# Optimization experiments

Measured on AMD Instinct MI355X. Metric: run time of the kernel, lower is better.

The kernel has to match this reference:

```python
import jax, jax.numpy as jnp
import numpy as np

N = 100000; S = 8; V = 10000; DE = 64; DH = 64; H = DH + 6; T = 2; E = 250000
MAXP = 10; SZ = 64; OUT = MAXP * SZ; NPLAIN = 6; NAR = 2


def setup_inputs() -> dict:
    key = jax.random.key(0)
    ks = jax.random.split(key, 20)
    rn = lambda k, sh, s=0.1: jax.random.normal(k, sh, jnp.float32) * s
    return {
        "tokens": jax.random.randint(ks[0], (N, S), 0, V, jnp.int32),
        "type_idx": jax.random.randint(ks[1], (N,), 0, 6, jnp.int32),
        "edge_src": jax.random.randint(ks[2], (T, E), 0, N, jnp.int32),
        "edge_dst": jax.random.randint(ks[3], (T, E), 0, N, jnp.int32),
        "map_entry_idx": 123,
        "embed": rn(ks[4], (V, DE), 0.3),
        "Wi_map": rn(ks[5], (3 * DH, DE)), "Wh_map": rn(ks[6], (3 * DH, DH)),
        "bi_map": jnp.zeros((3 * DH,), jnp.float32), "bh_map": jnp.zeros((3 * DH,), jnp.float32),
        "Wi_mem": rn(ks[7], (3 * DH, DE)), "Wh_mem": rn(ks[8], (3 * DH, DH)),
        "bi_mem": jnp.zeros((3 * DH,), jnp.float32), "bh_mem": jnp.zeros((3 * DH,), jnp.float32),
        "Wm_plain": rn(ks[9], (NPLAIN, T, H, H)), "bm_plain": jnp.zeros((NPLAIN, T, H), jnp.float32),
        "Wu_plain": rn(ks[10], (NPLAIN, 2 * H, H)), "bu_plain": jnp.zeros((NPLAIN, H), jnp.float32),
        "Wm_ar": rn(ks[11], (NAR, T, 2 * H, 2 * H)), "bm_ar": jnp.zeros((NAR, T, 2 * H), jnp.float32),
        "Wu_ar": rn(ks[12], (NAR, 4 * H, H)), "bu_ar": jnp.zeros((NAR, H), jnp.float32),
        "W1": rn(ks[13], (H, H)), "b1": jnp.zeros((H,), jnp.float32),
        "W2": rn(ks[14], (H, OUT)), "b2": jnp.zeros((OUT,), jnp.float32),
    }


def _gru_last(x_seq, Wi, Wh, bi, bh):
    # x_seq: [S, N, DE] -> last hidden [N, DH] (torch nn.GRU cell math)
    def step(h, x):
        gi = x @ Wi.T + bi
        gh = h @ Wh.T + bh
        ir, iz, inn = jnp.split(gi, 3, axis=-1)
        hr, hz, hn = jnp.split(gh, 3, axis=-1)
        r = jax.nn.sigmoid(ir + hr)
        z = jax.nn.sigmoid(iz + hz)
        n = jnp.tanh(inn + r * hn)
        return (1.0 - z) * n + z * h, None
    h0 = jnp.zeros((x_seq.shape[1], Wh.shape[1]), x_seq.dtype)
    h, _ = jax.lax.scan(step, h0, x_seq)
    return h


def _mp(h, src, dst, Wm, bm, Wu, bu, msg_act, dense_act):
    # per-edge-type linear message on sender state, scatter-max aggregation, dense update
    m = jnp.einsum('ted,tdm->tem', h[src], Wm) + bm[:, None, :]  # [T, E, M]
    if msg_act is not None:
        m = msg_act(m)
    agg = jax.ops.segment_max(m.reshape(-1, m.shape[-1]), dst.reshape(-1), num_segments=h.shape[0])
    agg = jnp.where(jnp.isneginf(agg), 0.0, agg)  # nodes with no incoming edges -> 0
    u = jnp.concatenate([h, agg], axis=-1) @ Wu + bu
    return dense_act(u) if dense_act is not None else u


def _forward(tokens, type_idx, edge_src, edge_dst, map_entry_idx, embed,
             Wi_map, Wh_map, bi_map, bh_map, Wi_mem, Wh_mem, bi_mem, bh_mem,
             Wm_plain, bm_plain, Wu_plain, bu_plain, Wm_ar, bm_ar, Wu_ar, bu_ar,
             W1, b1, W2, b2):
    x_seq = embed[tokens].transpose(1, 0, 2)  # [S, N, DE]
    h_map = _gru_last(x_seq, Wi_map, Wh_map, bi_map, bh_map)
    h_mem = _gru_last(x_seq, Wi_mem, Wh_mem, bi_mem, bh_mem)
    is_map = (type_idx == 0)[:, None]
    is_mem = (type_idx == 5)[:, None]
    node_h = jnp.where(is_map, h_map, jnp.where(is_mem, h_mem, 0.0))
    h = jnp.concatenate([jax.nn.one_hot(type_idx, 6, dtype=node_h.dtype), node_h], axis=-1)  # [N, H]
    li = 0
    for blk in range(2):  # two concat-residual blocks from create_mlp_mp_layers
        saved = h
        for _ in range(3):  # plain MLP MP layers: no msg/dense activation
            h = _mp(h, edge_src, edge_dst, Wm_plain[li], bm_plain[li], Wu_plain[li], bu_plain[li], None, None)
            li += 1
        h = jnp.concatenate([saved, h], axis=-1)  # ConcatResidualLayer -> [N, 2H]
        h = _mp(h, edge_src, edge_dst, Wm_ar[blk], bm_ar[blk], Wu_ar[blk], bu_ar[blk], jax.nn.gelu, jnp.tanh)
    x = h[map_entry_idx]            # select map entry node
    x = jax.nn.relu(x @ W1 + b1)    # trans_layers[0]
    return x @ W2 + b2


def reference(tokens, type_idx, edge_src, edge_dst, map_entry_idx, embed,
              Wi_map, Wh_map, bi_map, bh_map, Wi_mem, Wh_mem, bi_mem, bh_mem,
              Wm_plain, bm_plain, Wu_plain, bu_plain, Wm_ar, bm_ar, Wu_ar, bu_ar,
              W1, b1, W2, b2):
    return _forward(tokens, type_idx, edge_src, edge_dst, map_entry_idx, embed,
                    Wi_map, Wh_map, bi_map, bh_map, Wi_mem, Wh_mem, bi_mem, bh_mem,
                    Wm_plain, bm_plain, Wu_plain, bu_plain, Wm_ar, bm_ar, Wu_ar, bu_ar,
                    W1, b1, W2, b2)
```

## Files before the change

kernel.cpp:

```cpp
#include <hip/hip_runtime.h>
#include <math.h>

#define CAPT 20480
#define R2   (2*CAPT)
#define GLD  136
#define GRR  32

typedef __attribute__((ext_vector_type(8))) short short8;
typedef __attribute__((ext_vector_type(4))) float f32x4;

__device__ __forceinline__ float fexp2_(float x){ return __builtin_amdgcn_exp2f(x); }
__device__ __forceinline__ float frcp_(float x){ return __builtin_amdgcn_rcpf(x); }
__device__ __forceinline__ float ftanh_(float x){
  float ax = __builtin_fabsf(x);
  float t = fexp2_(-2.885390082f * ax);
  float r = (1.f - t) * frcp_(1.f + t);
  return __builtin_copysignf(r, x);
}
__device__ __forceinline__ float fsig_(float x){
  return frcp_(1.f + fexp2_(-1.442695041f * x));
}
__device__ __forceinline__ float fgelu_(float x){
  float x2 = x*x;
  float u  = x * __builtin_fmaf(x2, 0.044715f, 1.0f);
  float e  = fexp2_(u * -2.30220818f);
  return x * frcp_(1.f + e);
}
__device__ __forceinline__ unsigned short f2bf(float x){
  unsigned int u = __float_as_uint(x);
  return (unsigned short)((u + 0x7FFFu + ((u>>16)&1u)) >> 16);
}
__device__ __forceinline__ float bf2f(unsigned short v){
  return __uint_as_float(((unsigned int)v) << 16);
}
__device__ __forceinline__ unsigned int cvt_pk_bf16(float a, float b){
  unsigned int r;
  asm("v_cvt_pk_bf16_f32 %0, %1, %2" : "=v"(r) : "v"(a), "v"(b));
  return r;
}

__global__ void k_prepB(const float* __restrict__ Wm_plain, const float* __restrict__ Wu_plain,
                        const float* __restrict__ Wm_ar, const float* __restrict__ Wu_ar,
                        const float* __restrict__ Wi_map, const float* __restrict__ Wh_map,
                        const float* __restrict__ Wi_mem, const float* __restrict__ Wh_mem,
                        unsigned short* __restrict__ BtArena){
  int id = blockIdx.y;
  int Kp, elems, off;
  if (id < 6){ Kp=96;  elems=15360; off=id*15360; }
  else if (id < 12){ Kp=160; elems=12800; off=92160+(id-6)*12800; }
  else if (id < 14){ Kp=160; elems=51200; off=168960+(id-12)*51200; }
  else if (id < 16){ Kp=320; elems=25600; off=271360+(id-14)*25600; }
  else { Kp=128; elems=32768; off=322560+(id-16)*32768; }
  for (int g = blockIdx.x*256 + threadIdx.x; g < elems; g += 8*256){
    int c = g / Kp, k = g - c*Kp;
    float val = 0.f;
    if (id < 6){
      int li = id; int t = (c >= 80); int cc = c - t*80;
      if (cc < 70 && k < 70) val = Wm_plain[((li*2+t)*70 + k)*70 + cc];
    } else if (id < 12){
      int li = id-6;
      int kk = (k < 70) ? k : ((k >= 80 && k < 150) ? 70 + (k-80) : -1);
      if (c < 70 && kk >= 0) val = Wu_plain[(li*140 + kk)*70 + c];
    } else if (id < 14){
      int blk = id-12; int t = (c >= 160); int cc = c - t*160;
      int kk = (k < 70) ? k : ((k >= 80 && k < 150) ? 70 + (k-80) : -1);
      if (cc < 140 && kk >= 0) val = Wm_ar[(((blk*2+t)*140) + kk)*140 + cc];
    } else if (id < 16){
      int blk = id-14;
      int kk = (k < 70) ? k : ((k >= 80 && k < 150) ? 70 + (k-80)
               : ((k >= 160 && k < 300) ? 140 + (k-160) : -1));
      if (c < 70 && kk >= 0) val = Wu_ar[(blk*280 + kk)*70 + c];
    } else {
      int typ = id-16;
      const float* Wi = typ ? Wi_mem : Wi_map;
      const float* Wh = typ ? Wh_mem : Wh_map;
      if (c < 192) val = (k < 64) ? Wi[c*64 + k] : Wh[c*64 + (k-64)];
      else { int cc = c-192; val = (k >= 64) ? Wh[(128+cc)*64 + (k-64)] : 0.f; }
    }
    BtArena[off + g] = f2bf(val);
  }
}

__global__ void k_prepBias(const float* __restrict__ bm_plain, const float* __restrict__ bu_plain,
                           const float* __restrict__ bm_ar, const float* __restrict__ bu_ar,
                           const float* __restrict__ bi_map, const float* __restrict__ bh_map,
                           const float* __restrict__ bi_mem, const float* __restrict__ bh_mem,
                           float* __restrict__ biasA){
  for (int g = threadIdx.x; g < 2752; g += 256){
    float val = 0.f;
    if (g < 960){ int li=g/160, c=g%160; int t=(c>=80); int cc=c-t*80;
      if (cc<70) val = bm_plain[(li*2+t)*70 + cc]; }
    else if (g < 1440){ int u=g-960; int li=u/80, c=u%80; if (c<70) val = bu_plain[li*70+c]; }
    else if (g < 2080){ int u=g-1440; int blk=u/320, c=u%320; int t=(c>=160); int cc=c-t*160;
      if (cc<140) val = bm_ar[(blk*2+t)*140 + cc]; }
    else if (g < 2240){ int u=g-2080; int blk=u/80, c=u%80; if (c<70) val = bu_ar[blk*70+c]; }
    else { int u=g-2240; int typ=u/256, c=u%256;
      const float* bi = typ ? bi_mem : bi_map; const float* bh = typ ? bh_mem : bh_map;
      val = (c < 192) ? (bi[c]+bh[c]) : bh[128 + (c-192)]; }
    biasA[g] = val;
  }
}

__global__ void k_prepEmb(const float* __restrict__ embed, unsigned short* __restrict__ embB,
                          int total){
  int g = blockIdx.x*256 + threadIdx.x;
  if (g < total) embB[g] = f2bf(embed[g]);
}

__global__ void k_init_h(const int* __restrict__ type_idx, unsigned short* __restrict__ h, int N){
  int g = blockIdx.x*256 + threadIdx.x;
  if (g >= N*80) return;
  int n = g / 80, c = g - n*80;
  h[g] = (c < 6 && type_idx[n] == c) ? (unsigned short)0x3F80 : (unsigned short)0;
}

__global__ void k_compact(const int* __restrict__ type_idx, int* __restrict__ idxcat,
                          int* __restrict__ cnt, int N){
  int n = blockIdx.x*256 + threadIdx.x;
  if (n >= N) return;
  int t = type_idx[n];
  if (t == 0){ int p = atomicAdd(&cnt[0],1); if (p < CAPT) idxcat[p] = n; }
  else if (t == 5){ int p = atomicAdd(&cnt[1],1); if (p < CAPT) idxcat[CAPT+p] = n; }
}

__global__ void k_count(const int* __restrict__ edst, int* __restrict__ deg, int TE){
  int i = blockIdx.x*256 + threadIdx.x;
  if (i < TE) atomicAdd(&deg[edst[i]], 1);
}
__global__ void k_scan1(const int* __restrict__ deg, int* __restrict__ off,
                        int* __restrict__ bsum, int N){
  __shared__ int sh[256];
  int t = threadIdx.x; int base = blockIdx.x*2048;
  int v[8]; int s = 0;
  for (int i=0;i<8;i++){
    int g = base + t*8 + i;
    int x = (g<N)? (((deg[g]+3)>>2)<<2) : 0;
    v[i]=x; s+=x;
  }
  sh[t]=s; __syncthreads();
  for (int o=1;o<256;o<<=1){ int x = (t>=o)? sh[t-o]:0; __syncthreads(); sh[t]+=x; __syncthreads(); }
  if (t==255) bsum[blockIdx.x] = sh[255];
  int run = sh[t]-s;
  for (int i=0;i<8;i++){ int g = base + t*8 + i; if (g<N) off[g]=run; run+=v[i]; }
}
__global__ void k_scan2(int* bsum, int nb){
  if (threadIdx.x==0 && blockIdx.x==0){
    int run=0;
    for(int b=0;b<nb;b++){ int x=bsum[b]; bsum[b]=run; run+=x; }
    bsum[nb]=run;
  }
}
__global__ void k_scan3(int* __restrict__ off, const int* __restrict__ bsum, int N, int nb){
  int g = blockIdx.x*256+threadIdx.x;
  if (g < N) off[g] += bsum[g>>11];
  if (g == 0) off[N] = bsum[nb];
}
__global__ void k_fill(const int* __restrict__ esrc, const int* __restrict__ edst,
                       const int* __restrict__ off, int* __restrict__ cur,
                       int* __restrict__ edata, int TE, int E){
  int i = blockIdx.x*256 + threadIdx.x;
  if (i >= TE) return;
  int d = edst[i];
  int pos = off[d] + atomicAdd(&cur[d], 1);
  edata[pos] = (esrc[i] << 1) | (i >= E ? 1 : 0);
}
__global__ void k_pad(const int* __restrict__ off, const int* __restrict__ cur,
                      int* __restrict__ edata, int N){
  int n = blockIdx.x*256 + threadIdx.x;
  if (n >= N) return;
  int d = cur[n];
  if (d == 0) return;
  int d4 = ((d+3)>>2)<<2;
  int base = off[n];
  int first = edata[base];
  for (int i = d; i < d4; i++) edata[base+i] = first;
}

__global__ __launch_bounds__(256) void kgru(
    const int* __restrict__ idxcat, const int* __restrict__ tokens,
    const unsigned short* __restrict__ embB,
    const unsigned short* __restrict__ Bt, const unsigned short* __restrict__ Bt2,
    const float* __restrict__ bias, const float* __restrict__ bias2,
    unsigned short* __restrict__ hOut)
{
  __shared__ __align__(16) unsigned short As[2][GRR*GLD];
  __shared__ int tokS[GRR*8];
  __shared__ int idxS[GRR];
  int rb = blockIdx.y * CAPT + blockIdx.x * GRR;
  if (idxcat[rb] < 0) return;
  int t = threadIdx.x;
  int lane = t & 63, m = lane & 15, q = lane >> 4, w = t >> 6;
  const unsigned short* Bsel = blockIdx.y ? Bt2 : Bt;
  const float* bsel = blockIdx.y ? bias2 : bias;
  short8 breg[4][4]; float bv[4];
  #pragma unroll
  for (int j=0;j<4;j++){
    int col = (w + 4*j)*16 + m;
    bv[j] = bsel[col];
    #pragma unroll
    for (int kt=0;kt<4;kt++)
      breg[j][kt] = *(const short8*)&Bsel[(size_t)col*128 + kt*32 + q*8];
  }
  if (t < GRR) idxS[t] = idxcat[rb + t];
  if (t < GRR*8){
    int nd = idxcat[rb + (t>>3)]; if (nd < 0) nd = 0;
    tokS[t] = tokens[nd*8 + (t & 7)];
  }
  __syncthreads();
  if (t < GRR*8){
    int row = t >> 3, ch = t & 7;
    *(uint4*)&As[0][row*GLD + ch*8] = *(const uint4*)&embB[(size_t)tokS[row*8]*64 + ch*8];
  }
  for (int j = t; j < GRR*32; j += 256){
    int row = j >> 5, k2 = (j & 31)*2;
    *(unsigned int*)&As[0][row*GLD + 64 + k2] = 0;
  }
  __syncthreads();
  unsigned short hreg[2][4];
  #pragma unroll
  for (int rt=0;rt<2;rt++)
    #pragma unroll
    for (int i=0;i<4;i++) hreg[rt][i] = 0;
  int u = w*16 + m;
  int p = 0;
  for (int s = 0; s < 8; s++){
    uint4 xr;
    if (s < 7 && t < GRR*8){
      int row = t >> 3, ch = t & 7;
      xr = *(const uint4*)&embB[(size_t)tokS[row*8 + s + 1]*64 + ch*8];
    }
    f32x4 acc[2][4] = {};
    #pragma unroll
    for (int kt=0;kt<4;kt++){
      short8 af[2];
      #pragma unroll
      for (int rt=0;rt<2;rt++)
        af[rt] = *(const short8*)&As[p][(rt*16+m)*GLD + kt*32 + q*8];
      #pragma unroll
      for (int j=0;j<4;j++)
        #pragma unroll
        for (int rt=0;rt<2;rt++)
          acc[rt][j] = __builtin_amdgcn_mfma_f32_16x16x32_bf16(af[rt], breg[j][kt], acc[rt][j], 0,0,0);
    }
    #pragma unroll
    for (int rt=0;rt<2;rt++){
      float hv[4];
      #pragma unroll
      for (int i=0;i<4;i++){
        float rr = fsig_(acc[rt][0][i] + bv[0]);
        float zz = fsig_(acc[rt][1][i] + bv[1]);
        float hn = acc[rt][3][i] + bv[3];
        float nn = ftanh_(acc[rt][2][i] + bv[2] + (rr - 1.f)*hn);
        float hp = bf2f(hreg[rt][i]);
        hv[i] = (1.f - zz)*nn + zz*hp;
      }
      unsigned int plo = cvt_pk_bf16(hv[0], hv[1]);
      unsigned int phi = cvt_pk_bf16(hv[2], hv[3]);
      hreg[rt][0] = (unsigned short)plo;
      hreg[rt][1] = (unsigned short)(plo >> 16);
      hreg[rt][2] = (unsigned short)phi;
      hreg[rt][3] = (unsigned short)(phi >> 16);
    }
    if (s < 7){
      #pragma unroll
      for (int rt=0;rt<2;rt++)
        #pragma unroll
        for (int i=0;i<4;i++)
          As[p^1][(rt*16 + q*4 + i)*GLD + 64 + u] = hreg[rt][i];
      if (t < GRR*8){
        int row = t >> 3, ch = t & 7;
        *(uint4*)&As[p^1][row*GLD + ch*8] = xr;
      }
      __syncthreads();
      p ^= 1;
    } else {
      #pragma unroll
      for (int rt=0;rt<2;rt++)
        #pragma unroll
        for (int i=0;i<4;i++){
          int nd = idxS[rt*16 + q*4 + i];
          if (nd >= 0) hOut[(size_t)nd*80 + 6 + u] = hreg[rt][i];
        }
    }
  }
}

template<int RTR, int KT, int CT, int ACT>
__global__ __launch_bounds__(256) void wgemm(
    const unsigned short* __restrict__ A0, int w0, int ldA0,
    const unsigned short* __restrict__ A1, int w1, int ldA1,
    const unsigned short* __restrict__ A2, int w2, int ldA2,
    const unsigned short* __restrict__ Bt, int KpB,
    const float* __restrict__ bias,
    unsigned short* __restrict__ C, int ldC,
    int rows, int tiles)
{
  constexpr int Kpad = KT*32;
  constexpr int NRT  = RTR/16;
  constexpr int CPT  = (RTR*Kpad/8)/256;
  __shared__ __align__(16) unsigned short As[2][RTR*Kpad];
  int t = threadIdx.x;
  int lane = t & 63, m = lane & 15, q = lane >> 4, w = t >> 6;
  int tileBase = blockIdx.y * (4*CT);
  int rtEnd = (rows + RTR - 1)/RTR;
  int tr = blockIdx.x;
  if (tr >= rtEnd) return;

  short8 breg[CT][KT]; float bv[CT]; bool val[CT]; int colr[CT];
  #pragma unroll
  for (int j=0;j<CT;j++){
    int tt = tileBase + w + 4*j;
    val[j] = (tt < tiles);
    int col = tt*16 + m;
    colr[j] = col;
    bv[j] = 0.f;
    if (val[j]){
      bv[j] = bias[col];
      #pragma unroll
      for (int kt=0;kt<KT;kt++)
        breg[j][kt] = *(const short8*)&Bt[(size_t)col*KpB + kt*32 + q*8];
    } else {
      #pragma unroll
      for (int kt=0;kt<KT;kt++) breg[j][kt] = (short8){0,0,0,0,0,0,0,0};
    }
  }

  int w01 = w0 + w1, w012 = w0 + w1 + w2;
  uint4 r[CPT];
  auto loadRegs = [&](int trr){
    #pragma unroll
    for (int i=0;i<CPT;i++){
      int c = i*256 + t;
      int row = c / (KT*4), kc = (c - row*(KT*4))*8;
      int gr = trr*RTR + row;
      uint4 v = {0,0,0,0};
      if (gr < rows && kc < w012){
        const unsigned short* sp;
        if (kc < w0)       sp = A0 + (size_t)gr*ldA0 + kc;
        else if (kc < w01) sp = A1 + (size_t)gr*ldA1 + (kc - w0);
        else               sp = A2 + (size_t)gr*ldA2 + (kc - w01);
        v = *(const uint4*)sp;
      }
      r[i] = v;
    }
  };
  auto dsw = [&](int p){
    #pragma unroll
    for (int i=0;i<CPT;i++){
      int c = i*256 + t;
      int row = c / (KT*4), ch = c - row*(KT*4);
      int phys = ch ^ (row & 3);
      *(uint4*)&As[p][row*Kpad + phys*8] = r[i];
    }
  };

  loadRegs(tr);
  dsw(0);
  int p = 0;
  for (;;){
    int nxt = tr + gridDim.x;
    bool hasNext = (nxt < rtEnd);
    if (hasNext) loadRegs(nxt);
    __syncthreads();
    f32x4 acc[NRT][CT] = {};
    #pragma unroll
    for (int kt=0;kt<KT;kt++){
      short8 af[NRT];
      #pragma unroll
      for (int rt=0;rt<NRT;rt++)
        af[rt] = *(const short8*)&As[p][(rt*16+m)*Kpad + (((kt*4+q) ^ (m&3))*8)];
      #pragma unroll
      for (int j=0;j<CT;j++)
        #pragma unroll
        for (int rt=0;rt<NRT;rt++)
          acc[rt][j] = __builtin_amdgcn_mfma_f32_16x16x32_bf16(af[rt], breg[j][kt], acc[rt][j], 0,0,0);
    }
    bool tfull = (tr*RTR + RTR <= rows);
#define EPILOG(CHK)                                                         \
    _Pragma("unroll")                                                       \
    for (int rt=0;rt<NRT;rt++){                                             \
      int rbase = tr*RTR + rt*16 + q*4;                                     \
      _Pragma("unroll")                                                     \
      for (int j=0;j<CT;j++){                                               \
        if (!val[j]) continue;                                              \
        float v0 = acc[rt][j][0] + bv[j];                                   \
        float v1 = acc[rt][j][1] + bv[j];                                   \
        float v2 = acc[rt][j][2] + bv[j];                                   \
        float v3 = acc[rt][j][3] + bv[j];                                   \
        if (ACT == 1){ v0=fgelu_(v0); v1=fgelu_(v1); v2=fgelu_(v2); v3=fgelu_(v3); } \
        else if (ACT == 2){ v0=ftanh_(v0); v1=ftanh_(v1); v2=ftanh_(v2); v3=ftanh_(v3); } \
        unsigned int plo = cvt_pk_bf16(v0, v1);                             \
        unsigned int phi = cvt_pk_bf16(v2, v3);                             \
        size_t cb = (size_t)rbase*ldC + colr[j];                            \
        if (!CHK || rbase+0 < rows) C[cb]           = (unsigned short)plo;         \
        if (!CHK || rbase+1 < rows) C[cb + ldC]     = (unsigned short)(plo >> 16); \
        if (!CHK || rbase+2 < rows) C[cb + 2*ldC]   = (unsigned short)phi;         \
        if (!CHK || rbase+3 < rows) C[cb + 3*ldC]   = (unsigned short)(phi >> 16); \
      }                                                                     \
    }
    if (tfull){ EPILOG(false) } else { EPILOG(true) }
#undef EPILOG
    if (!hasNext) break;
    dsw(p^1);
    p ^= 1; tr = nxt;
  }
}

__global__ __launch_bounds__(256) void k_aggregate(
    const int* __restrict__ off, const int* __restrict__ edata,
    const unsigned short* __restrict__ P2, int ldP, int off1,
    unsigned short* __restrict__ agg, int M, int N, int WPN)
{
  int t = threadIdx.x;
  int lane = t & 63, w = t >> 6;
  int nbase, c;
  if (WPN == 1){
    nbase = blockIdx.x*16 + w*4;
    c = 2*lane;
  } else {
    nbase = blockIdx.x*8 + (w>>1)*4;
    c = (w & 1)*80 + 2*lane;
  }
  nbase = __builtin_amdgcn_readfirstlane(nbase);
  if (nbase >= N) return;
  bool act = (lane < 40);
  const float NEG = -__builtin_inff();
  int e[4], e1[4];
  float f0[4], f1[4];
  #pragma unroll
  for (int j=0;j<4;j++){
    int n = nbase + j;
    bool v = (n < N);
    e[j]  = v ? __builtin_amdgcn_readfirstlane(off[n])     : 0;
    e1[j] = v ? __builtin_amdgcn_readfirstlane(off[n + 1]) : 0;
    f0[j] = NEG; f1[j] = NEG;
  }
  for (;;){
    bool cond[4];
    bool any = false;
    #pragma unroll
    for (int j=0;j<4;j++){ cond[j] = (e[j] < e1[j]); any |= cond[j]; }
    if (!any) break;
    unsigned int rr[4][4];
    #pragma unroll
    for (int j=0;j<4;j++){
      if (cond[j]){
        int4 g = *(const int4*)&edata[e[j]];
        int b0 = (g.x>>1)*ldP + (g.x&1)*off1;
        int b1 = (g.y>>1)*ldP + (g.y&1)*off1;
        int b2 = (g.z>>1)*ldP + (g.z&1)*off1;
        int b3 = (g.w>>1)*ldP + (g.w&1)*off1;
        if (act){
          rr[j][0] = *(const unsigned int*)(P2 + b0 + c);
          rr[j][1] = *(const unsigned int*)(P2 + b1 + c);
          rr[j][2] = *(const unsigned int*)(P2 + b2 + c);
          rr[j][3] = *(const unsigned int*)(P2 + b3 + c);
        }
      }
    }
    #pragma unroll
    for (int j=0;j<4;j++){
      if (cond[j]){
        if (act){
          unsigned int u0 = rr[j][0], u1 = rr[j][1], u2 = rr[j][2], u3 = rr[j][3];
          f0[j] = fmaxf(f0[j], fmaxf(fmaxf(__uint_as_float(u0<<16), __uint_as_float(u1<<16)),
                                     fmaxf(__uint_as_float(u2<<16), __uint_as_float(u3<<16))));
          f1[j] = fmaxf(f1[j], fmaxf(fmaxf(__uint_as_float(u0&0xFFFF0000u), __uint_as_float(u1&0xFFFF0000u)),
                                     fmaxf(__uint_as_float(u2&0xFFFF0000u), __uint_as_float(u3&0xFFFF0000u))));
        }
        e[j] += 4;
      }
    }
  }
  if (act){
    #pragma unroll
    for (int j=0;j<4;j++){
      int n = nbase + j;
      if (n >= N) continue;
      unsigned int o = (__float_as_uint(f0[j] == NEG ? 0.f : f0[j]) >> 16)
                     |  (__float_as_uint(f1[j] == NEG ? 0.f : f1[j]) & 0xFFFF0000u);
      *(unsigned int*)(agg + (size_t)n*M + c) = o;
    }
  }
}

__global__ void k_head(const unsigned short* __restrict__ h, const int* __restrict__ entry,
                       const float* __restrict__ W1, const float* __restrict__ b1,
                       const float* __restrict__ W2, const float* __restrict__ b2,
                       float* __restrict__ out){
  __shared__ float x[70], x1[70];
  int t = threadIdx.x;
  if (t < 70) x[t] = bf2f(h[(size_t)(*entry)*80 + t]);
  __syncthreads();
  if (t < 70){
    float s = b1[t];
    for (int i=0;i<70;i++) s += x[i]*W1[i*70 + t];
    x1[t] = fmaxf(s, 0.f);
  }
  __syncthreads();
  if (t < 640){
    float s = b2[t];
    for (int i=0;i<70;i++) s += x1[i]*W2[i*640 + t];
    out[t] = s;
  }
}

extern "C" void kernel_launch(void* const* d_in, const int* in_sizes, int n_in,
                              void* d_out, int out_size, void* d_ws, size_t ws_size,
                              hipStream_t stream) {
  const int*   tokens   = (const int*)d_in[0];
  const int*   type_idx = (const int*)d_in[1];
  const int*   esrc     = (const int*)d_in[2];
  const int*   edst     = (const int*)d_in[3];
  const int*   entry    = (const int*)d_in[4];
  const float* embed    = (const float*)d_in[5];
  const float* Wi_map   = (const float*)d_in[6];
  const float* Wh_map   = (const float*)d_in[7];
  const float* bi_map   = (const float*)d_in[8];
  const float* bh_map   = (const float*)d_in[9];
  const float* Wi_mem   = (const float*)d_in[10];
  const float* Wh_mem   = (const float*)d_in[11];
  const float* bi_mem   = (const float*)d_in[12];
  const float* bh_mem   = (const float*)d_in[13];
  const float* Wm_plain = (const float*)d_in[14];
  const float* bm_plain = (const float*)d_in[15];
  const float* Wu_plain = (const float*)d_in[16];
  const float* bu_plain = (const float*)d_in[17];
  const float* Wm_ar    = (const float*)d_in[18];
  const float* bm_ar    = (const float*)d_in[19];
  const float* Wu_ar    = (const float*)d_in[20];
  const float* bu_ar    = (const float*)d_in[21];
  const float* W1 = (const float*)d_in[22];
  const float* b1 = (const float*)d_in[23];
  const float* W2 = (const float*)d_in[24];
  const float* b2 = (const float*)d_in[25];
  float* out = (float*)d_out;

  const int N  = in_sizes[1];
  const int TE = in_sizes[2];
  const int E  = TE / 2;
  const int V64 = in_sizes[5];

  char* p = (char*)d_ws;
  auto alloc = [&](size_t bytes)->char* { char* r = p; p += (bytes + 255) & ~(size_t)255; return r; };
  unsigned short* hA  = (unsigned short*)alloc((size_t)N*80*2);
  unsigned short* hB  = (unsigned short*)alloc((size_t)N*80*2);
  unsigned short* hC  = (unsigned short*)alloc((size_t)N*80*2);
  unsigned short* P2  = (unsigned short*)alloc((size_t)N*320*2);
  unsigned short* agg = (unsigned short*)alloc((size_t)N*160*2);
  int* deg    = (int*)alloc((size_t)N*4);
  int* curp   = (int*)alloc((size_t)N*4);
  int* off    = (int*)alloc((size_t)(N+8)*4);
  int* edata  = (int*)alloc((size_t)(TE + 4*N + 16)*4);
  int* sbsum  = (int*)alloc(256*4);
  int* cnt    = (int*)alloc(16*4);
  int* idxcat = (int*)alloc((size_t)R2*4);
  unsigned short* BtA  = (unsigned short*)alloc(388096*2);
  float* biasA = (float*)alloc(2752*4);
  unsigned short* embB = (unsigned short*)alloc((size_t)V64*2);

  hipMemsetAsync(idxcat, 0xFF, (size_t)R2*4, stream);
  hipMemsetAsync(cnt,    0,    16*4, stream);
  hipMemsetAsync(deg,    0,    (size_t)N*4, stream);
  hipMemsetAsync(curp,   0,    (size_t)N*4, stream);

  k_prepB<<<dim3(8,18), 256, 0, stream>>>(Wm_plain, Wu_plain, Wm_ar, Wu_ar,
                                          Wi_map, Wh_map, Wi_mem, Wh_mem, BtA);
  k_prepBias<<<1, 256, 0, stream>>>(bm_plain, bu_plain, bm_ar, bu_ar,
                                    bi_map, bh_map, bi_mem, bh_mem, biasA);
  k_prepEmb<<<(V64+255)/256, 256, 0, stream>>>(embed, embB, V64);
  k_init_h<<<(N*80+255)/256, 256, 0, stream>>>(type_idx, hA, N);
  k_compact<<<(N+255)/256, 256, 0, stream>>>(type_idx, idxcat, cnt, N);

  k_count<<<(TE+255)/256, 256, 0, stream>>>(edst, deg, TE);
  int nb = (N + 2047)/2048;
  k_scan1<<<nb, 256, 0, stream>>>(deg, off, sbsum, N);
  k_scan2<<<1, 64, 0, stream>>>(sbsum, nb);
  k_scan3<<<(N+255)/256, 256, 0, stream>>>(off, sbsum, N, nb);
  k_fill<<<(TE+255)/256, 256, 0, stream>>>(esrc, edst, off, curp, edata, TE, E);
  k_pad<<<(N+255)/256, 256, 0, stream>>>(off, curp, edata, N);

  kgru<<<dim3(CAPT/GRR, 2), 256, 0, stream>>>(
      idxcat, tokens, embB,
      BtA + 322560, BtA + 322560 + 32768,
      biasA + 2240, biasA + 2240 + 256, hA);

  unsigned short* cur = hA; unsigned short* f1 = hB; unsigned short* f2 = hC;
  int li = 0;
  for (int blk = 0; blk < 2; blk++){
    unsigned short* saved = cur;
    unsigned short* ins[3]  = {cur, f1, f2};
    unsigned short* outs[3] = {f1, f2, f1};
    for (int j = 0; j < 3; j++){
      unsigned short* X = ins[j]; unsigned short* Yo = outs[j];
      wgemm<64,3,3,0><<<dim3(1024,1), 256, 0, stream>>>(
          X, 80, 80,  nullptr, 0, 0,  nullptr, 0, 0,
          BtA + li*15360, 96, biasA + li*160,
          P2, 160, N, 10);
      k_aggregate<<<(N+15)/16, 256, 0, stream>>>(off, edata, P2, 160, 80, agg, 80, N, 1);
      wgemm<64,5,2,0><<<dim3(1024,1), 256, 0, stream>>>(
          X, 80, 80,  agg, 80, 80,  nullptr, 0, 0,
          BtA + 92160 + li*12800, 160, biasA + 960 + li*80,
          Yo, 80, N, 5);
      li++;
    }
    wgemm<64,5,3,1><<<dim3(512,2), 256, 0, stream>>>(
        saved, 80, 80,  f1, 80, 80,  nullptr, 0, 0,
        BtA + 168960 + blk*51200, 160, biasA + 1440 + blk*320,
        P2, 320, N, 20);
    k_aggregate<<<(N+7)/8, 256, 0, stream>>>(off, edata, P2, 320, 160, agg, 160, N, 2);
    wgemm<32,10,2,2><<<dim3(1024,1), 256, 0, stream>>>(
        saved, 80, 80,  f1, 80, 80,  agg, 160, 160,
        BtA + 271360 + blk*25600, 320, biasA + 2080 + blk*80,
        f2, 80, N, 5);
    unsigned short* t3 = cur; cur = f2; f2 = t3;
  }

  k_head<<<1, 640, 0, stream>>>(cur, entry, W1, b1, W2, b2, out);
}
```

Before: 760.3 us.

## Replace persistent double-buffered wgemm with one-tile-per-block launch; simplify GRU activations

The wgemm kernels are no longer persistent: instead of a fixed grid looping over row tiles with register prefetch and double-buffered LDS, each block now handles exactly one row tile and the grid is sized to the number of tiles. This removes the loop, the second LDS buffer and the prefetch logic, and relies on hardware scheduling across many more blocks to hide load latency. The cost is reloading the B-weight registers in every block. Separately, tanh is rewritten as 1-2/(1+e^{2x}) and the GRU gate math is reorganised into FMAs with a folded (r-1) term, which removes a few ALU ops but may lose some accuracy or saturate differently for large inputs.

```diff
diff --git a/kernel.cpp b/kernel.cpp
--- a/kernel.cpp
+++ b/kernel.cpp
@@ -12,10 +12,8 @@
 __device__ __forceinline__ float fexp2_(float x){ return __builtin_amdgcn_exp2f(x); }
 __device__ __forceinline__ float frcp_(float x){ return __builtin_amdgcn_rcpf(x); }
 __device__ __forceinline__ float ftanh_(float x){
-  float ax = __builtin_fabsf(x);
-  float t = fexp2_(-2.885390082f * ax);
-  float r = (1.f - t) * frcp_(1.f + t);
-  return __builtin_copysignf(r, x);
+  float t = fexp2_(2.885390082f * x);
+  return __builtin_fmaf(-2.f, frcp_(1.f + t), 1.f);
 }
 __device__ __forceinline__ float fsig_(float x){
   return frcp_(1.f + fexp2_(-1.442695041f * x));
@@ -247,12 +245,16 @@
       float hv[4];
       #pragma unroll
       for (int i=0;i<4;i++){
-        float rr = fsig_(acc[rt][0][i] + bv[0]);
-        float zz = fsig_(acc[rt][1][i] + bv[1]);
-        float hn = acc[rt][3][i] + bv[3];
-        float nn = ftanh_(acc[rt][2][i] + bv[2] + (rr - 1.f)*hn);
+        float xrg = acc[rt][0][i] + bv[0];
+        float xzg = acc[rt][1][i] + bv[1];
+        float xng = acc[rt][2][i] + bv[2];
+        float hng = acc[rt][3][i] + bv[3];
+        float pm = frcp_(1.f + fexp2_(1.442695041f*xrg));
+        float zz = frcp_(1.f + fexp2_(-1.442695041f*xzg));
+        float a  = __builtin_fmaf(-pm, hng, xng);
+        float th = ftanh_(a);
         float hp = bf2f(hreg[rt][i]);
-        hv[i] = (1.f - zz)*nn + zz*hp;
+        hv[i] = __builtin_fmaf(zz, hp - th, th);
       }
       unsigned int plo = cvt_pk_bf16(hv[0], hv[1]);
       unsigned int phi = cvt_pk_bf16(hv[2], hv[3]);
@@ -298,7 +300,7 @@
   constexpr int Kpad = KT*32;
   constexpr int NRT  = RTR/16;
   constexpr int CPT  = (RTR*Kpad/8)/256;
-  __shared__ __align__(16) unsigned short As[2][RTR*Kpad];
+  __shared__ __align__(16) unsigned short As[RTR*Kpad];
   int t = threadIdx.x;
   int lane = t & 63, m = lane & 15, q = lane >> 4, w = t >> 6;
   int tileBase = blockIdx.y * (4*CT);
@@ -327,55 +329,44 @@
 
   int w01 = w0 + w1, w012 = w0 + w1 + w2;
   uint4 r[CPT];
-  auto loadRegs = [&](int trr){
-    #pragma unroll
-    for (int i=0;i<CPT;i++){
-      int c = i*256 + t;
-      int row = c / (KT*4), kc = (c - row*(KT*4))*8;
-      int gr = trr*RTR + row;
-      uint4 v = {0,0,0,0};
-      if (gr < rows && kc < w012){
-        const unsigned short* sp;
-        if (kc < w0)       sp = A0 + (size_t)gr*ldA0 + kc;
-        else if (kc < w01) sp = A1 + (size_t)gr*ldA1 + (kc - w0);
-        else               sp = A2 + (size_t)gr*ldA2 + (kc - w01);
-        v = *(const uint4*)sp;
-      }
-      r[i] = v;
-    }
-  };
-  auto dsw = [&](int p){
-    #pragma unroll
-    for (int i=0;i<CPT;i++){
-      int c = i*256 + t;
-      int row = c / (KT*4), ch = c - row*(KT*4);
-      int phys = ch ^ (row & 3);
-      *(uint4*)&As[p][row*Kpad + phys*8] = r[i];
-    }
-  };
-
-  loadRegs(tr);
-  dsw(0);
-  int p = 0;
-  for (;;){
-    int nxt = tr + gridDim.x;
-    bool hasNext = (nxt < rtEnd);
-    if (hasNext) loadRegs(nxt);
-    __syncthreads();
-    f32x4 acc[NRT][CT] = {};
-    #pragma unroll
-    for (int kt=0;kt<KT;kt++){
-      short8 af[NRT];
+  #pragma unroll
+  for (int i=0;i<CPT;i++){
+    int c = i*256 + t;
+    int row = c / (KT*4), kc = (c - row*(KT*4))*8;
+    int gr = tr*RTR + row;
+    uint4 v = {0,0,0,0};
+    if (gr < rows && kc < w012){
+      const unsigned short* sp;
+      if (kc < w0)       sp = A0 + (size_t)gr*ldA0 + kc;
+      else if (kc < w01) sp = A1 + (size_t)gr*ldA1 + (kc - w0);
+      else               sp = A2 + (size_t)gr*ldA2 + (kc - w01);
+      v = *(const uint4*)sp;
+    }
+    r[i] = v;
+  }
+  #pragma unroll
+  for (int i=0;i<CPT;i++){
+    int c = i*256 + t;
+    int row = c / (KT*4), ch = c - row*(KT*4);
+    int phys = ch ^ (row & 3);
+    *(uint4*)&As[row*Kpad + phys*8] = r[i];
+  }
+  __syncthreads();
+
+  f32x4 acc[NRT][CT] = {};
+  #pragma unroll
+  for (int kt=0;kt<KT;kt++){
+    short8 af[NRT];
+    #pragma unroll
+    for (int rt=0;rt<NRT;rt++)
+      af[rt] = *(const short8*)&As[(rt*16+m)*Kpad + (((kt*4+q) ^ (m&3))*8)];
+    #pragma unroll
+    for (int j=0;j<CT;j++)
       #pragma unroll
       for (int rt=0;rt<NRT;rt++)
-        af[rt] = *(const short8*)&As[p][(rt*16+m)*Kpad + (((kt*4+q) ^ (m&3))*8)];
-      #pragma unroll
-      for (int j=0;j<CT;j++)
-        #pragma unroll
-        for (int rt=0;rt<NRT;rt++)
-          acc[rt][j] = __builtin_amdgcn_mfma_f32_16x16x32_bf16(af[rt], breg[j][kt], acc[rt][j], 0,0,0);
-    }
-    bool tfull = (tr*RTR + RTR <= rows);
+        acc[rt][j] = __builtin_amdgcn_mfma_f32_16x16x32_bf16(af[rt], breg[j][kt], acc[rt][j], 0,0,0);
+  }
+  bool tfull = (tr*RTR + RTR <= rows);
 #define EPILOG(CHK)                                                         \
     _Pragma("unroll")                                                       \
     for (int rt=0;rt<NRT;rt++){                                             \
@@ -398,12 +389,8 @@
         if (!CHK || rbase+3 < rows) C[cb + 3*ldC]   = (unsigned short)(phi >> 16); \
       }                                                                     \
     }
-    if (tfull){ EPILOG(false) } else { EPILOG(true) }
+  if (tfull){ EPILOG(false) } else { EPILOG(true) }
 #undef EPILOG
-    if (!hasNext) break;
-    dsw(p^1);
-    p ^= 1; tr = nxt;
-  }
 }
 
 __global__ __launch_bounds__(256) void k_aggregate(
@@ -585,6 +572,9 @@
       BtA + 322560, BtA + 322560 + 32768,
       biasA + 2240, biasA + 2240 + 256, hA);
 
+  const int T64 = (N + 63)/64;
+  const int T32 = (N + 31)/32;
+
   unsigned short* cur = hA; unsigned short* f1 = hB; unsigned short* f2 = hC;
   int li = 0;
   for (int blk = 0; blk < 2; blk++){
@@ -593,23 +583,23 @@
     unsigned short* outs[3] = {f1, f2, f1};
     for (int j = 0; j < 3; j++){
       unsigned short* X = ins[j]; unsigned short* Yo = outs[j];
-      wgemm<64,3,3,0><<<dim3(1024,1), 256, 0, stream>>>(
+      wgemm<64,3,3,0><<<dim3(T64,1), 256, 0, stream>>>(
           X, 80, 80,  nullptr, 0, 0,  nullptr, 0, 0,
           BtA + li*15360, 96, biasA + li*160,
           P2, 160, N, 10);
       k_aggregate<<<(N+15)/16, 256, 0, stream>>>(off, edata, P2, 160, 80, agg, 80, N, 1);
-      wgemm<64,5,2,0><<<dim3(1024,1), 256, 0, stream>>>(
+      wgemm<64,5,2,0><<<dim3(T64,1), 256, 0, stream>>>(
           X, 80, 80,  agg, 80, 80,  nullptr, 0, 0,
           BtA + 92160 + li*12800, 160, biasA + 960 + li*80,
           Yo, 80, N, 5);
       li++;
     }
-    wgemm<64,5,3,1><<<dim3(512,2), 256, 0, stream>>>(
+    wgemm<64,5,3,1><<<dim3(T64,2), 256, 0, stream>>>(
         saved, 80, 80,  f1, 80, 80,  nullptr, 0, 0,
         BtA + 168960 + blk*51200, 160, biasA + 1440 + blk*320,
         P2, 320, N, 20);
     k_aggregate<<<(N+7)/8, 256, 0, stream>>>(off, edata, P2, 320, 160, agg, 160, N, 2);
-    wgemm<32,10,2,2><<<dim3(1024,1), 256, 0, stream>>>(
+    wgemm<32,10,2,2><<<dim3(T32,1), 256, 0, stream>>>(
         saved, 80, 80,  f1, 80, 80,  agg, 160, 160,
         BtA + 271360 + blk*25600, 320, biasA + 2080 + blk*80,
         f2, 80, N, 5);
```

Measured after the change: 779.2 us. +2.5%, slower.
